# Kernel tuning notes

Hardware: AMD Instinct MI355X
Metric: run time of the kernel (lower is better)

## Reference

```python
import jax, jax.numpy as jnp
import numpy as np

B, S, D, H, E = 4, 2048, 256, 8, 65536
HD = D // H  # head_dim = 32


def _layernorm(x, g, b, eps=1e-5):
    mu = jnp.mean(x, axis=-1, keepdims=True)
    var = jnp.var(x, axis=-1, keepdims=True)
    return (x - mu) * jax.lax.rsqrt(var + eps) * g + b


def setup_inputs() -> dict:
    key = jax.random.key(0)
    ks = jax.random.split(key, 16)
    sd = 1.0 / np.sqrt(D)
    inp = {
        "x": jax.random.normal(ks[0], (B, S, D), jnp.float32),
        "adj_mask": jax.random.uniform(ks[1], (B, S, S)) < 0.05,  # ~32 neighbors/node
        "edge_attr": jax.random.normal(ks[2], (E,), jnp.float32),
        "edge_index": jax.random.randint(ks[3], (2, E), 0, S),
        "ln1_g": jnp.ones((D,), jnp.float32),
        "ln1_b": jnp.zeros((D,), jnp.float32),
        "wq": jax.random.normal(ks[4], (D, D), jnp.float32) * sd,
        "bq": jnp.zeros((D,), jnp.float32),
        "wk": jax.random.normal(ks[5], (D, D), jnp.float32) * sd,
        "bk": jnp.zeros((D,), jnp.float32),
        "wv": jax.random.normal(ks[6], (D, D), jnp.float32) * sd,
        "bv": jnp.zeros((D,), jnp.float32),
        "wo": jax.random.normal(ks[7], (D, D), jnp.float32) * sd,
        "bo": jnp.zeros((D,), jnp.float32),
        "ln2_g": jnp.ones((D,), jnp.float32),
        "ln2_b": jnp.zeros((D,), jnp.float32),
        "w1": jax.random.normal(ks[8], (4 * D, D), jnp.float32) * sd,
        "b1": jnp.zeros((4 * D,), jnp.float32),
        "w2": jax.random.normal(ks[9], (D, 4 * D), jnp.float32) * (1.0 / np.sqrt(4 * D)),
        "b2": jnp.zeros((D,), jnp.float32),
    }
    return inp


def reference(x, adj_mask, edge_attr, edge_index,
              ln1_g, ln1_b, wq, bq, wk, bk, wv, bv, wo, bo,
              ln2_g, ln2_b, w1, b1, w2, b2):
    residual = x
    nx = _layernorm(x, ln1_g, ln1_b)
    # projections (torch Linear: y = x W^T + b)
    q = nx @ wq.T + bq
    k = nx @ wk.T + bk
    v = nx @ wv.T + bv
    # (B,S,D) -> (B,H,S,HD)
    q = q.reshape(B, S, H, HD).transpose(0, 2, 1, 3)
    k = k.reshape(B, S, H, HD).transpose(0, 2, 1, 3)
    v = v.reshape(B, S, H, HD).transpose(0, 2, 1, 3)
    scores = jnp.einsum("bhqd,bhkd->bhqk", q, k) / np.sqrt(HD)
    scores = jnp.where(adj_mask[:, None, :, :], scores, -1e9)
    # edge-attr bias: scatter clipped attr into (S,S), gated per-batch by adj_mask,
    # broadcast over heads (replaces the nested python loop)
    clipped = jnp.clip(edge_attr, -5.0, 5.0)
    bias2d = jnp.zeros((S, S), scores.dtype).at[edge_index[0], edge_index[1]].set(clipped)
    scores = scores + jnp.where(adj_mask, bias2d[None, :, :], 0.0)[:, None, :, :]
    attn = jax.nn.softmax(scores, axis=-1)
    ctx = jnp.einsum("bhqk,bhkd->bhqd", attn, v)
    ctx = ctx.transpose(0, 2, 1, 3).reshape(B, S, D)
    x = residual + (ctx @ wo.T + bo)
    # MLP block (exact GELU, like torch nn.GELU())
    n2 = _layernorm(x, ln2_g, ln2_b)
    h = jax.nn.gelu(n2 @ w1.T + b1, approximate=False)
    x = x + (h @ w2.T + b2)
    return x
```

## Files before the change

### kernel.cpp

```cpp
#include <hip/hip_runtime.h>
#include <stdint.h>

#define S 2048
#define D 256
#define H 8
#define HD 32
#define E_EDGES 65536
#define DFF 1024
#define M_TOK 8192
#define CAP 512
#define QKVN 768

typedef __attribute__((ext_vector_type(8))) short s16x8;
typedef __attribute__((ext_vector_type(8))) unsigned short u16x8;
typedef __attribute__((ext_vector_type(4))) unsigned short u16x4v;
typedef __attribute__((ext_vector_type(4))) float f32x4;

__device__ __forceinline__ float b2f(unsigned short u){
  union { unsigned int i; float f; } x; x.i = ((unsigned int)u) << 16; return x.f;
}
__device__ __forceinline__ unsigned short f2b(float f){
  union { float f; unsigned int i; } x; x.f = f;
  unsigned int r = x.i + 0x7fffu + ((x.i >> 16) & 1u);
  return (unsigned short)(r >> 16);
}
__device__ __forceinline__ void gload_lds16(const void* g, void* l) {
  __builtin_amdgcn_global_load_lds(
      (const __attribute__((address_space(1))) unsigned int*)g,
      (__attribute__((address_space(3))) unsigned int*)l, 16, 0, 0);
}

__global__ __launch_bounds__(256) void prep_kernel(
    const float* __restrict__ wq, const float* __restrict__ wk,
    const float* __restrict__ wv, const float* __restrict__ wo,
    const float* __restrict__ w1, const float* __restrict__ w2,
    const float* __restrict__ bq, const float* __restrict__ bk,
    const float* __restrict__ bv,
    unsigned short* __restrict__ wqkvb, unsigned short* __restrict__ wob,
    unsigned short* __restrict__ w1b, unsigned short* __restrict__ w2b,
    float* __restrict__ bqkv)
{
  const int i = blockIdx.x * 256 + threadIdx.x;
  const float* src; unsigned short* dst; int off;
  if      (i <  16384) { src = wq; dst = wqkvb;            off = i; }
  else if (i <  32768) { src = wk; dst = wqkvb +  65536;   off = i -  16384; }
  else if (i <  49152) { src = wv; dst = wqkvb + 131072;   off = i -  32768; }
  else if (i <  65536) { src = wo; dst = wob;              off = i -  49152; }
  else if (i < 131072) { src = w1; dst = w1b;              off = i -  65536; }
  else                 { src = w2; dst = w2b;              off = i - 131072; }
  const float4 v = ((const float4*)src)[off];
  unsigned short o[4] = { f2b(v.x), f2b(v.y), f2b(v.z), f2b(v.w) };
  *(uint2*)(dst + (size_t)off * 4) = *(const uint2*)o;
  if      (i <  64) ((float4*)bqkv)[i]       = ((const float4*)bq)[i];
  else if (i < 128) ((float4*)bqkv)[i - 64]  = ((const float4*)bk)[i - 64],  ((float4*)bqkv)[i] = ((const float4*)bk)[i - 64];
}

__global__ __launch_bounds__(192) void bias_kernel(
    const float* __restrict__ bq, const float* __restrict__ bk,
    const float* __restrict__ bv, float* __restrict__ bqkv)
{
  const int i = threadIdx.x;
  if      (i <  64) ((float4*)bqkv)[i] = ((const float4*)bq)[i];
  else if (i < 128) ((float4*)bqkv)[i] = ((const float4*)bk)[i - 64];
  else              ((float4*)bqkv)[i] = ((const float4*)bv)[i - 128];
}

__global__ __launch_bounds__(256) void ln_kernel(
    const float* __restrict__ xf,
    const float* __restrict__ g, const float* __restrict__ bt,
    unsigned short* __restrict__ out)
{
  const int wave = threadIdx.x >> 6;
  const int lane = threadIdx.x & 63;
  const int row = blockIdx.x * 4 + wave;
  const size_t base = (size_t)row * D + lane * 4;
  const float4 u = *(const float4*)(xf + base);
  float v[4] = { u.x, u.y, u.z, u.w };
  float s  = v[0]+v[1]+v[2]+v[3];
  float s2 = v[0]*v[0]+v[1]*v[1]+v[2]*v[2]+v[3]*v[3];
  #pragma unroll
  for (int off=32; off>=1; off>>=1){ s += __shfl_xor(s,off,64); s2 += __shfl_xor(s2,off,64); }
  const float mu  = s * (1.f/D);
  const float var = s2 * (1.f/D) - mu*mu;
  const float rs  = 1.f / sqrtf(var + 1e-5f);
  #pragma unroll
  for (int j=0;j<4;++j){
    const int c = lane*4 + j;
    const float y = (v[j]-mu)*rs*g[c] + bt[c];
    out[(size_t)row*D + c] = f2b(y);
  }
}

template<int BM, int BN, int WR, int WC>
__global__ __launch_bounds__(256) void gemm_lds(
    const unsigned short* __restrict__ A,
    const unsigned short* __restrict__ W,
    const float* __restrict__ bias,
    unsigned short* __restrict__ outb,
    float* __restrict__ outf,
    const float* __restrict__ resf,
    int M, int N, int K, int act)
{
  constexpr int WM = BM / WR, WN = BN / WC;
  constexpr int MI = WM / 16, NI = WN / 16;
  __shared__ unsigned short As[2][BM * 32];
  __shared__ unsigned short Bs[2][BN * 32];
  const int tid  = threadIdx.x;
  const int wave = tid >> 6;
  const int lane = tid & 63;
  const int wr = wave / WC, wc = wave % WC;
  const int m0 = blockIdx.y * BM;
  const int n0 = blockIdx.x * BN;
  const int ldr = lane >> 2;
  const int ldc = (lane & 3) * 8;
  const int fr = lane & 15;
  const int kf = (lane >> 4) * 8;
  f32x4 acc[MI][NI];
  #pragma unroll
  for (int i=0;i<MI;++i)
    #pragma unroll
    for (int j=0;j<NI;++j)
      #pragma unroll
      for (int r=0;r<4;++r) acc[i][j][r] = 0.f;

  auto stage = [&](int buf, int k0) {
    #pragma unroll
    for (int c = wave; c < BM/16; c += 4)
      gload_lds16(A + (size_t)(m0 + c*16 + ldr)*K + k0 + ldc, &As[buf][c*512]);
    #pragma unroll
    for (int c = wave; c < BN/16; c += 4)
      gload_lds16(W + (size_t)(n0 + c*16 + ldr)*K + k0 + ldc, &Bs[buf][c*512]);
  };

  stage(0, 0);
  __syncthreads();
  int cur = 0;
  for (int k0 = 0; k0 < K; k0 += 32) {
    if (k0 + 32 < K) stage(cur ^ 1, k0 + 32);
    s16x8 af[MI], bf[NI];
    #pragma unroll
    for (int i = 0; i < MI; ++i) af[i] = *(const s16x8*)&As[cur][(wr*WM + i*16 + fr)*32 + kf];
    #pragma unroll
    for (int j = 0; j < NI; ++j) bf[j] = *(const s16x8*)&Bs[cur][(wc*WN + j*16 + fr)*32 + kf];
    #pragma unroll
    for (int i = 0; i < MI; ++i)
      #pragma unroll
      for (int j = 0; j < NI; ++j)
        acc[i][j] = __builtin_amdgcn_mfma_f32_16x16x32_bf16(af[i], bf[j], acc[i][j], 0, 0, 0);
    __syncthreads();
    cur ^= 1;
  }
  const int rbase = (lane >> 4) * 4;
  #pragma unroll
  for (int j = 0; j < NI; ++j) {
    const int col = n0 + wc*WN + j*16 + fr;
    const float bvl = bias[col];
    #pragma unroll
    for (int i = 0; i < MI; ++i) {
      #pragma unroll
      for (int r = 0; r < 4; ++r) {
        const int row = m0 + wr*WM + i*16 + rbase + r;
        const size_t off = (size_t)row * N + col;
        float vv = acc[i][j][r] + bvl;
        if (act) vv = 0.5f * vv * (1.0f + erff(vv * 0.70710678118654752f));
        if (resf) vv += resf[off];
        if (outb) outb[off] = f2b(vv);
        if (outf) outf[off] = vv;
      }
    }
  }
}

__global__ __launch_bounds__(256) void zero_kernel(uint4* __restrict__ p, int n4) {
  int i = blockIdx.x * 256 + threadIdx.x;
  if (i < n4) { uint4 z; z.x=0; z.y=0; z.z=0; z.w=0; p[i] = z; }
}
__global__ __launch_bounds__(256) void scatter_kernel(
    const int* __restrict__ ei, const float* __restrict__ attr,
    unsigned int* __restrict__ packed)
{
  int e = blockIdx.x * 256 + threadIdx.x;
  if (e >= E_EDGES) return;
  int r = ei[e], c = ei[E_EDGES + e];
  float v = attr[e];
  v = fminf(5.f, fmaxf(-5.f, v));
  unsigned int pk = (((unsigned int)e) << 16) | (unsigned int)f2b(v);
  atomicMax(&packed[(size_t)r * S + c], pk);
}

__global__ __launch_bounds__(256) void attn_kernel(
    const unsigned short* __restrict__ qkv,
    const int* __restrict__ mask,
    const unsigned int* __restrict__ packed,
    unsigned short* __restrict__ ctx)
{
  __shared__ unsigned short nidx[CAP];
  __shared__ float nbias[CAP];
  __shared__ float sc[CAP*9];
  __shared__ float qs[D];
  __shared__ float red[4*D];
  __shared__ float rsum[H];
  __shared__ int wtot[4], wbase[4], cnt_s;
  const int t = threadIdx.x;
  const int wave = t >> 6, lane = t & 63;
  const int bqi = blockIdx.x;
  const int b = bqi >> 11;
  const int qrow = bqi & (S-1);
  qs[t] = b2f(qkv[(size_t)bqi * QKVN + t]);

  const int* mrow = mask + (size_t)bqi * S;
  const uint4 ma = *(const uint4*)(mrow + t*8);
  const uint4 mb = *(const uint4*)(mrow + t*8 + 4);
  unsigned int mv[8] = { ma.x, ma.y, ma.z, ma.w, mb.x, mb.y, mb.z, mb.w };
  int mycnt = 0;
  #pragma unroll
  for (int j = 0; j < 8; ++j) mycnt += mv[j] ? 1 : 0;
  int inc = mycnt;
  #pragma unroll
  for (int off=1; off<64; off<<=1){ int y = __shfl_up(inc, off, 64); if (lane >= off) inc += y; }
  if (lane == 63) wtot[wave] = inc;
  __syncthreads();
  if (t == 0) { int ss=0; for (int w=0; w<4; ++w){ wbase[w]=ss; ss+=wtot[w]; } cnt_s = ss; }
  __syncthreads();
  int pos = wbase[wave] + inc - mycnt;
  #pragma unroll
  for (int j = 0; j < 8; ++j) {
    if (mv[j]) {
      if (pos < CAP) nidx[pos] = (unsigned short)(t*8 + j);
      ++pos;
    }
  }
  __syncthreads();
  int cnt = cnt_s; if (cnt > CAP) cnt = CAP;
  const int cnt_pad = (cnt + 31) & ~31;
  for (int i = cnt + t; i < cnt_pad; i += 256) nidx[i] = 0;

  for (int i = t; i < cnt; i += 256) {
    unsigned int pkv = packed[(size_t)qrow * S + nidx[i]];
    nbias[i] = b2f((unsigned short)(pkv & 0xffffu));
  }
  __syncthreads();

  const int hh = lane >> 3;
  const int d4 = (lane & 7) * 4;
  const float scale = 0.17677669529663687f;
  float q4[4];
  #pragma unroll
  for (int j = 0; j < 4; ++j) q4[j] = qs[hh*HD + d4 + j];
  const size_t rowbase = (size_t)b * S * QKVN;

  for (int n0 = wave*8; n0 < cnt_pad; n0 += 32) {
    u16x4v kv[8];
    #pragma unroll
    for (int u = 0; u < 8; ++u)
      kv[u] = *(const u16x4v*)(qkv + rowbase + (size_t)nidx[n0+u]*QKVN + 256 + lane*4);
    #pragma unroll
    for (int u = 0; u < 8; ++u) {
      float p = q4[0]*b2f(kv[u][0]) + q4[1]*b2f(kv[u][1]) + q4[2]*b2f(kv[u][2]) + q4[3]*b2f(kv[u][3]);
      p += __shfl_xor(p, 1, 64);
      p += __shfl_xor(p, 2, 64);
      p += __shfl_xor(p, 4, 64);
      if ((lane & 7) == 0) {
        const int n = n0 + u;
        sc[n*9 + hh] = (n < cnt) ? p * scale + nbias[n] : 0.f;
      }
    }
  }
  __syncthreads();

  if (cnt > 0) {
    const int h = t >> 5, dd = t & 31;
    float m = -1e30f;
    for (int n = dd; n < cnt; n += 32) m = fmaxf(m, sc[n*9 + h]);
    #pragma unroll
    for (int off=16; off>=1; off>>=1) m = fmaxf(m, __shfl_xor(m, off, 64));
    float sum = 0.f;
    for (int n = dd; n < cnt; n += 32) {
      float e = __expf(sc[n*9 + h] - m);
      sc[n*9 + h] = e;
      sum += e;
    }
    #pragma unroll
    for (int off=16; off>=1; off>>=1) sum += __shfl_xor(sum, off, 64);
    if (dd == 0) rsum[h] = 1.f / sum;
  }
  __syncthreads();

  float a4[4] = {0.f, 0.f, 0.f, 0.f};
  if (cnt > 0) {
    for (int n0 = wave*8; n0 < cnt_pad; n0 += 32) {
      u16x4v vv[8];
      #pragma unroll
      for (int u = 0; u < 8; ++u)
        vv[u] = *(const u16x4v*)(qkv + rowbase + (size_t)nidx[n0+u]*QKVN + 512 + lane*4);
      #pragma unroll
      for (int u = 0; u < 8; ++u) {
        const float p = sc[(n0+u)*9 + hh];
        a4[0] += p * b2f(vv[u][0]);
        a4[1] += p * b2f(vv[u][1]);
        a4[2] += p * b2f(vv[u][2]);
        a4[3] += p * b2f(vv[u][3]);
      }
    }
    const float rinv = rsum[hh];
    #pragma unroll
    for (int j = 0; j < 4; ++j) a4[j] *= rinv;
  } else {
    for (int n = wave; n < S; n += 4) {
      const unsigned short* vrow = qkv + rowbase + (size_t)n * QKVN + 512;
      u16x4v vv = *(const u16x4v*)(vrow + lane*4);
      a4[0] += b2f(vv[0]); a4[1] += b2f(vv[1]); a4[2] += b2f(vv[2]); a4[3] += b2f(vv[3]);
    }
    #pragma unroll
    for (int j = 0; j < 4; ++j) a4[j] *= (1.f / S);
  }
  #pragma unroll
  for (int j = 0; j < 4; ++j) red[wave*D + lane*4 + j] = a4[j];
  __syncthreads();
  float outv = red[t] + red[D + t] + red[2*D + t] + red[3*D + t];
  ctx[(size_t)bqi * D + t] = f2b(outv);
}

extern "C" void kernel_launch(void* const* d_in, const int* in_sizes, int n_in,
                              void* d_out, int out_size, void* d_ws, size_t ws_size,
                              hipStream_t stream) {
  const float*          x    = (const float*)d_in[0];
  const int*            mask = (const int*)d_in[1];
  const float*          eat  = (const float*)d_in[2];
  const int*            eidx = (const int*)d_in[3];
  const float*          ln1g = (const float*)d_in[4];
  const float*          ln1b = (const float*)d_in[5];
  const float*          wq   = (const float*)d_in[6];
  const float*          bq   = (const float*)d_in[7];
  const float*          wk   = (const float*)d_in[8];
  const float*          bk   = (const float*)d_in[9];
  const float*          wv   = (const float*)d_in[10];
  const float*          bv   = (const float*)d_in[11];
  const float*          wo   = (const float*)d_in[12];
  const float*          bo   = (const float*)d_in[13];
  const float*          ln2g = (const float*)d_in[14];
  const float*          ln2b = (const float*)d_in[15];
  const float*          w1   = (const float*)d_in[16];
  const float*          b1   = (const float*)d_in[17];
  const float*          w2   = (const float*)d_in[18];
  const float*          b2   = (const float*)d_in[19];
  float* out = (float*)d_out;

  char* ws = (char*)d_ws;
  unsigned short* nx   = (unsigned short*)ws;
  unsigned short* qkv  = nx + (size_t)M_TOK*D;
  unsigned short* cx   = qkv + (size_t)M_TOK*QKVN;
  float*          x1   = (float*)(cx + (size_t)M_TOK*D);
  unsigned int*   pk   = (unsigned int*)(x1 + (size_t)M_TOK*D);
  unsigned short* wqkvb= (unsigned short*)(pk + (size_t)S*S);
  unsigned short* wob  = wqkvb + (size_t)QKVN*D;
  unsigned short* w1b  = wob + (size_t)D*D;
  unsigned short* w2b  = w1b + (size_t)DFF*D;
  float*          bqkv = (float*)(w2b + (size_t)D*DFF);
  unsigned short* hb   = qkv;
  unsigned short* n2   = nx;

  prep_kernel<<<768, 256, 0, stream>>>(wq, wk, wv, wo, w1, w2, bq, bk, bv,
                                       wqkvb, wob, w1b, w2b, bqkv);
  bias_kernel<<<1, 192, 0, stream>>>(bq, bk, bv, bqkv);
  zero_kernel<<<(S*S/4 + 255)/256, 256, 0, stream>>>((uint4*)pk, S*S/4);
  scatter_kernel<<<E_EDGES/256, 256, 0, stream>>>(eidx, eat, pk);
  ln_kernel<<<M_TOK/4, 256, 0, stream>>>(x, ln1g, ln1b, nx);
  gemm_lds<64,128,1,4><<<dim3(QKVN/128, M_TOK/64), 256, 0, stream>>>(nx, wqkvb, bqkv, qkv, nullptr, nullptr, M_TOK, QKVN, D, 0);
  attn_kernel<<<M_TOK, 256, 0, stream>>>(qkv, mask, pk, cx);
  gemm_lds<64,64,2,2><<<dim3(D/64, M_TOK/64), 256, 0, stream>>>(cx, wob, bo, nullptr, x1, x, M_TOK, D, D, 0);
  ln_kernel<<<M_TOK/4, 256, 0, stream>>>(x1, ln2g, ln2b, n2);
  gemm_lds<128,128,2,2><<<dim3(DFF/128, M_TOK/128), 256, 0, stream>>>(n2, w1b, b1, hb, nullptr, nullptr, M_TOK, DFF, D, 1);
  gemm_lds<64,64,2,2><<<dim3(D/64, M_TOK/64), 256, 0, stream>>>(hb, w2b, b2, nullptr, out, x1, M_TOK, D, DFF, 0);
}
```

Before: 177.6 us.

## Remap attention lanes to neighbor-by-head with per-thread full head dot products

Changes the attention thread mapping so each lane handles one neighbor and one head, doing a full 32-element dot product with 16-byte K/V loads instead of 4-element partials followed by shuffle reductions. Precomputed byte offsets per neighbor are stored in shared memory, and the PV accumulation keeps 32 accumulators per lane, reduced with cross-lane shuffles at the end. Softmax normalization moves to the final output sum. This also drops the redundant bias copy from the prep kernel. It trades shuffle and score-store overhead for higher register use (q32 and a32 arrays), which may lower occupancy, plus a 32-step shuffle reduction.

```diff
diff --git a/kernel.cpp b/kernel.cpp
--- a/kernel.cpp
+++ b/kernel.cpp
@@ -34,11 +34,8 @@
     const float* __restrict__ wq, const float* __restrict__ wk,
     const float* __restrict__ wv, const float* __restrict__ wo,
     const float* __restrict__ w1, const float* __restrict__ w2,
-    const float* __restrict__ bq, const float* __restrict__ bk,
-    const float* __restrict__ bv,
     unsigned short* __restrict__ wqkvb, unsigned short* __restrict__ wob,
-    unsigned short* __restrict__ w1b, unsigned short* __restrict__ w2b,
-    float* __restrict__ bqkv)
+    unsigned short* __restrict__ w1b, unsigned short* __restrict__ w2b)
 {
   const int i = blockIdx.x * 256 + threadIdx.x;
   const float* src; unsigned short* dst; int off;
@@ -51,8 +48,6 @@
   const float4 v = ((const float4*)src)[off];
   unsigned short o[4] = { f2b(v.x), f2b(v.y), f2b(v.z), f2b(v.w) };
   *(uint2*)(dst + (size_t)off * 4) = *(const uint2*)o;
-  if      (i <  64) ((float4*)bqkv)[i]       = ((const float4*)bq)[i];
-  else if (i < 128) ((float4*)bqkv)[i - 64]  = ((const float4*)bk)[i - 64],  ((float4*)bqkv)[i] = ((const float4*)bk)[i - 64];
 }
 
 __global__ __launch_bounds__(192) void bias_kernel(
@@ -195,9 +190,9 @@
     unsigned short* __restrict__ ctx)
 {
   __shared__ unsigned short nidx[CAP];
+  __shared__ unsigned int noff[CAP];
   __shared__ float nbias[CAP];
   __shared__ float sc[CAP*9];
-  __shared__ float qs[D];
   __shared__ float red[4*D];
   __shared__ float rsum[H];
   __shared__ int wtot[4], wbase[4], cnt_s;
@@ -206,7 +201,6 @@
   const int bqi = blockIdx.x;
   const int b = bqi >> 11;
   const int qrow = bqi & (S-1);
-  qs[t] = b2f(qkv[(size_t)bqi * QKVN + t]);
 
   const int* mrow = mask + (size_t)bqi * S;
   const uint4 ma = *(const uint4*)(mrow + t*8);
@@ -233,38 +227,47 @@
   __syncthreads();
   int cnt = cnt_s; if (cnt > CAP) cnt = CAP;
   const int cnt_pad = (cnt + 31) & ~31;
-  for (int i = cnt + t; i < cnt_pad; i += 256) nidx[i] = 0;
+  for (int i = cnt + t; i < cnt_pad; i += 256) { nidx[i] = 0; noff[i] = 512u; nbias[i] = 0.f; }
 
   for (int i = t; i < cnt; i += 256) {
-    unsigned int pkv = packed[(size_t)qrow * S + nidx[i]];
+    const unsigned int ni = nidx[i];
+    noff[i] = ni * 1536u + 512u;
+    unsigned int pkv = packed[(size_t)qrow * S + ni];
     nbias[i] = b2f((unsigned short)(pkv & 0xffffu));
   }
   __syncthreads();
 
-  const int hh = lane >> 3;
-  const int d4 = (lane & 7) * 4;
+  const int ns = lane >> 3;
+  const int hh = lane & 7;
   const float scale = 0.17677669529663687f;
-  float q4[4];
-  #pragma unroll
-  for (int j = 0; j < 4; ++j) q4[j] = qs[hh*HD + d4 + j];
-  const size_t rowbase = (size_t)b * S * QKVN;
+  const char* kbase = (const char*)(qkv + (size_t)b * S * QKVN) + hh * 64;
+
+  float q32[32];
+  {
+    const u16x8* qp = (const u16x8*)(qkv + (size_t)bqi * QKVN + hh * HD);
+    #pragma unroll
+    for (int c = 0; c < 4; ++c) {
+      u16x8 qv = qp[c];
+      #pragma unroll
+      for (int j = 0; j < 8; ++j) q32[c*8+j] = b2f(qv[j]);
+    }
+  }
 
   for (int n0 = wave*8; n0 < cnt_pad; n0 += 32) {
-    u16x4v kv[8];
-    #pragma unroll
-    for (int u = 0; u < 8; ++u)
-      kv[u] = *(const u16x4v*)(qkv + rowbase + (size_t)nidx[n0+u]*QKVN + 256 + lane*4);
-    #pragma unroll
-    for (int u = 0; u < 8; ++u) {
-      float p = q4[0]*b2f(kv[u][0]) + q4[1]*b2f(kv[u][1]) + q4[2]*b2f(kv[u][2]) + q4[3]*b2f(kv[u][3]);
-      p += __shfl_xor(p, 1, 64);
-      p += __shfl_xor(p, 2, 64);
-      p += __shfl_xor(p, 4, 64);
-      if ((lane & 7) == 0) {
-        const int n = n0 + u;
-        sc[n*9 + hh] = (n < cnt) ? p * scale + nbias[n] : 0.f;
-      }
-    }
+    const int n = n0 + ns;
+    const unsigned int off = noff[n];
+    const u16x8* kp = (const u16x8*)(kbase + off);
+    u16x8 kv0 = kp[0], kv1 = kp[1], kv2 = kp[2], kv3 = kp[3];
+    float d0 = 0.f, d1 = 0.f, d2 = 0.f, d3 = 0.f;
+    #pragma unroll
+    for (int j = 0; j < 8; ++j) {
+      d0 += q32[j]    * b2f(kv0[j]);
+      d1 += q32[8+j]  * b2f(kv1[j]);
+      d2 += q32[16+j] * b2f(kv2[j]);
+      d3 += q32[24+j] * b2f(kv3[j]);
+    }
+    const float scv = ((d0+d1)+(d2+d3)) * scale + nbias[n];
+    sc[n*9 + hh] = (n < cnt) ? scv : 0.f;
   }
   __syncthreads();
 
@@ -286,38 +289,48 @@
   }
   __syncthreads();
 
-  float a4[4] = {0.f, 0.f, 0.f, 0.f};
   if (cnt > 0) {
+    float a32[32];
+    #pragma unroll
+    for (int j = 0; j < 32; ++j) a32[j] = 0.f;
     for (int n0 = wave*8; n0 < cnt_pad; n0 += 32) {
-      u16x4v vv[8];
-      #pragma unroll
-      for (int u = 0; u < 8; ++u)
-        vv[u] = *(const u16x4v*)(qkv + rowbase + (size_t)nidx[n0+u]*QKVN + 512 + lane*4);
-      #pragma unroll
-      for (int u = 0; u < 8; ++u) {
-        const float p = sc[(n0+u)*9 + hh];
-        a4[0] += p * b2f(vv[u][0]);
-        a4[1] += p * b2f(vv[u][1]);
-        a4[2] += p * b2f(vv[u][2]);
-        a4[3] += p * b2f(vv[u][3]);
+      const int n = n0 + ns;
+      const unsigned int off = noff[n];
+      const u16x8* vp = (const u16x8*)(kbase + off + 512);
+      u16x8 v0 = vp[0], v1 = vp[1], v2 = vp[2], v3 = vp[3];
+      const float p = sc[n*9 + hh];
+      #pragma unroll
+      for (int j = 0; j < 8; ++j) {
+        a32[j]    += p * b2f(v0[j]);
+        a32[8+j]  += p * b2f(v1[j]);
+        a32[16+j] += p * b2f(v2[j]);
+        a32[24+j] += p * b2f(v3[j]);
       }
     }
-    const float rinv = rsum[hh];
-    #pragma unroll
-    for (int j = 0; j < 4; ++j) a4[j] *= rinv;
+    #pragma unroll
+    for (int mm = 8; mm <= 32; mm <<= 1)
+      #pragma unroll
+      for (int j = 0; j < 32; ++j) a32[j] += __shfl_xor(a32[j], mm, 64);
+    if (ns == 0) {
+      #pragma unroll
+      for (int c = 0; c < 8; ++c) {
+        f32x4 w4 = { a32[c*4], a32[c*4+1], a32[c*4+2], a32[c*4+3] };
+        *(f32x4*)&red[wave*D + hh*HD + c*4] = w4;
+      }
+    }
   } else {
+    float a4[4] = {0.f, 0.f, 0.f, 0.f};
     for (int n = wave; n < S; n += 4) {
-      const unsigned short* vrow = qkv + rowbase + (size_t)n * QKVN + 512;
-      u16x4v vv = *(const u16x4v*)(vrow + lane*4);
+      const u16x4v vv = *(const u16x4v*)((const char*)(qkv + (size_t)b*S*QKVN) + (size_t)n*1536 + 1024 + lane*8);
       a4[0] += b2f(vv[0]); a4[1] += b2f(vv[1]); a4[2] += b2f(vv[2]); a4[3] += b2f(vv[3]);
     }
     #pragma unroll
     for (int j = 0; j < 4; ++j) a4[j] *= (1.f / S);
-  }
-  #pragma unroll
-  for (int j = 0; j < 4; ++j) red[wave*D + lane*4 + j] = a4[j];
-  __syncthreads();
-  float outv = red[t] + red[D + t] + red[2*D + t] + red[3*D + t];
+    *(f32x4*)&red[wave*D + lane*4] = *(f32x4*)a4;
+    if (t < 8) rsum[t] = 1.f;
+  }
+  __syncthreads();
+  const float outv = (red[t] + red[D + t] + red[2*D + t] + red[3*D + t]) * rsum[t >> 5];
   ctx[(size_t)bqi * D + t] = f2b(outv);
 }
 
@@ -360,8 +373,7 @@
   unsigned short* hb   = qkv;
   unsigned short* n2   = nx;
 
-  prep_kernel<<<768, 256, 0, stream>>>(wq, wk, wv, wo, w1, w2, bq, bk, bv,
-                                       wqkvb, wob, w1b, w2b, bqkv);
+  prep_kernel<<<768, 256, 0, stream>>>(wq, wk, wv, wo, w1, w2, wqkvb, wob, w1b, w2b);
   bias_kernel<<<1, 192, 0, stream>>>(bq, bk, bv, bqkv);
   zero_kernel<<<(S*S/4 + 255)/256, 256, 0, stream>>>((uint4*)pk, S*S/4);
   scatter_kernel<<<E_EDGES/256, 256, 0, stream>>>(eidx, eat, pk);
```

Result: slower. 187.2 us (+5.4%).

## Split neighbor-list build into CSR kernel and store K/V as fp32 rows

Applied to the files above, without the earlier changes.

Moves mask compaction and edge-bias lookup out of the attention kernel into a separate csr_kernel that writes packed (index, bias) entries per query. The QKV GEMM now writes Q as bf16 and K/V as fp32 into separate buffers, so attention reads 16-byte float4 gathers with no bf16 conversion. Neighbor capacity drops from 512 to 192, which shrinks shared memory and should raise occupancy, but it truncates any row with more than 192 neighbors. The workspace is reorganized with aliased buffers, and the fp32 K/V doubles gather bandwidth per neighbor.

```diff
diff --git a/kernel.cpp b/kernel.cpp
--- a/kernel.cpp
+++ b/kernel.cpp
@@ -8,7 +8,7 @@
 #define E_EDGES 65536
 #define DFF 1024
 #define M_TOK 8192
-#define CAP 512
+#define CAPR 192
 #define QKVN 768
 
 typedef __attribute__((ext_vector_type(8))) short s16x8;
@@ -34,11 +34,8 @@
     const float* __restrict__ wq, const float* __restrict__ wk,
     const float* __restrict__ wv, const float* __restrict__ wo,
     const float* __restrict__ w1, const float* __restrict__ w2,
-    const float* __restrict__ bq, const float* __restrict__ bk,
-    const float* __restrict__ bv,
     unsigned short* __restrict__ wqkvb, unsigned short* __restrict__ wob,
-    unsigned short* __restrict__ w1b, unsigned short* __restrict__ w2b,
-    float* __restrict__ bqkv)
+    unsigned short* __restrict__ w1b, unsigned short* __restrict__ w2b)
 {
   const int i = blockIdx.x * 256 + threadIdx.x;
   const float* src; unsigned short* dst; int off;
@@ -51,8 +48,6 @@
   const float4 v = ((const float4*)src)[off];
   unsigned short o[4] = { f2b(v.x), f2b(v.y), f2b(v.z), f2b(v.w) };
   *(uint2*)(dst + (size_t)off * 4) = *(const uint2*)o;
-  if      (i <  64) ((float4*)bqkv)[i]       = ((const float4*)bq)[i];
-  else if (i < 128) ((float4*)bqkv)[i - 64]  = ((const float4*)bk)[i - 64],  ((float4*)bqkv)[i] = ((const float4*)bk)[i - 64];
 }
 
 __global__ __launch_bounds__(192) void bias_kernel(
@@ -96,8 +91,9 @@
     const unsigned short* __restrict__ A,
     const unsigned short* __restrict__ W,
     const float* __restrict__ bias,
-    unsigned short* __restrict__ outb,
+    unsigned short* __restrict__ outb, int obN,
     float* __restrict__ outf,
+    float* __restrict__ outkv,
     const float* __restrict__ resf,
     int M, int N, int K, int act)
 {
@@ -164,8 +160,9 @@
         float vv = acc[i][j][r] + bvl;
         if (act) vv = 0.5f * vv * (1.0f + erff(vv * 0.70710678118654752f));
         if (resf) vv += resf[off];
-        if (outb) outb[off] = f2b(vv);
+        if (outb && col < obN) outb[(size_t)row * obN + col] = f2b(vv);
         if (outf) outf[off] = vv;
+        if (outkv && col >= 256) outkv[(size_t)row * 512 + (col - 256)] = vv;
       }
     }
   }
@@ -188,26 +185,16 @@
   atomicMax(&packed[(size_t)r * S + c], pk);
 }
 
-__global__ __launch_bounds__(256) void attn_kernel(
-    const unsigned short* __restrict__ qkv,
-    const int* __restrict__ mask,
-    const unsigned int* __restrict__ packed,
-    unsigned short* __restrict__ ctx)
-{
-  __shared__ unsigned short nidx[CAP];
-  __shared__ float nbias[CAP];
-  __shared__ float sc[CAP*9];
-  __shared__ float qs[D];
-  __shared__ float red[4*D];
-  __shared__ float rsum[H];
+__global__ __launch_bounds__(256) void csr_kernel(
+    const int* __restrict__ mask, const unsigned int* __restrict__ packed,
+    unsigned int* __restrict__ csr, int* __restrict__ cnts)
+{
+  __shared__ unsigned short nidx[CAPR];
   __shared__ int wtot[4], wbase[4], cnt_s;
   const int t = threadIdx.x;
   const int wave = t >> 6, lane = t & 63;
   const int bqi = blockIdx.x;
-  const int b = bqi >> 11;
   const int qrow = bqi & (S-1);
-  qs[t] = b2f(qkv[(size_t)bqi * QKVN + t]);
-
   const int* mrow = mask + (size_t)bqi * S;
   const uint4 ma = *(const uint4*)(mrow + t*8);
   const uint4 mb = *(const uint4*)(mrow + t*8 + 4);
@@ -226,43 +213,71 @@
   #pragma unroll
   for (int j = 0; j < 8; ++j) {
     if (mv[j]) {
-      if (pos < CAP) nidx[pos] = (unsigned short)(t*8 + j);
+      if (pos < CAPR) nidx[pos] = (unsigned short)(t*8 + j);
       ++pos;
     }
   }
   __syncthreads();
-  int cnt = cnt_s; if (cnt > CAP) cnt = CAP;
+  int cnt = cnt_s; if (cnt > CAPR) cnt = CAPR;
   const int cnt_pad = (cnt + 31) & ~31;
-  for (int i = cnt + t; i < cnt_pad; i += 256) nidx[i] = 0;
-
-  for (int i = t; i < cnt; i += 256) {
-    unsigned int pkv = packed[(size_t)qrow * S + nidx[i]];
-    nbias[i] = b2f((unsigned short)(pkv & 0xffffu));
-  }
-  __syncthreads();
+  for (int i = t; i < cnt_pad; i += 256) {
+    unsigned int e = 0;
+    if (i < cnt) {
+      const unsigned int ni = nidx[i];
+      e = (ni << 16) | (packed[(size_t)qrow * S + ni] & 0xffffu);
+    }
+    csr[(size_t)bqi * CAPR + i] = e;
+  }
+  if (t == 0) cnts[bqi] = cnt;
+}
+
+__global__ __launch_bounds__(256) void attn_kernel(
+    const unsigned short* __restrict__ qb,
+    const float* __restrict__ kvf,
+    const unsigned int* __restrict__ csr,
+    const int* __restrict__ cnts,
+    unsigned short* __restrict__ ctx)
+{
+  __shared__ unsigned int nle[CAPR];
+  __shared__ float sc[CAPR*9];
+  __shared__ float red[4*D];
+  __shared__ float rsum[H];
+  const int t = threadIdx.x;
+  const int wave = t >> 6, lane = t & 63;
+  const int bqi = blockIdx.x;
+  const int b = bqi >> 11;
+  const char* kvb = (const char*)(kvf + (size_t)b * S * 512);
+
+  const int cnt = cnts[bqi];
+  const int cnt_pad = (cnt + 31) & ~31;
+  for (int i = t; i < cnt_pad; i += 256) nle[i] = csr[(size_t)bqi * CAPR + i];
 
   const int hh = lane >> 3;
-  const int d4 = (lane & 7) * 4;
   const float scale = 0.17677669529663687f;
   float q4[4];
-  #pragma unroll
-  for (int j = 0; j < 4; ++j) q4[j] = qs[hh*HD + d4 + j];
-  const size_t rowbase = (size_t)b * S * QKVN;
+  {
+    const u16x4v qv = *(const u16x4v*)(qb + (size_t)bqi * D + lane * 4);
+    #pragma unroll
+    for (int j = 0; j < 4; ++j) q4[j] = b2f(qv[j]);
+  }
+  __syncthreads();
 
   for (int n0 = wave*8; n0 < cnt_pad; n0 += 32) {
-    u16x4v kv[8];
+    unsigned int e[8]; float4 kv[8];
+    #pragma unroll
+    for (int u = 0; u < 8; ++u) e[u] = nle[n0 + u];
     #pragma unroll
     for (int u = 0; u < 8; ++u)
-      kv[u] = *(const u16x4v*)(qkv + rowbase + (size_t)nidx[n0+u]*QKVN + 256 + lane*4);
+      kv[u] = *(const float4*)(kvb + (size_t)((e[u] >> 16) * 2048u) + lane*16);
     #pragma unroll
     for (int u = 0; u < 8; ++u) {
-      float p = q4[0]*b2f(kv[u][0]) + q4[1]*b2f(kv[u][1]) + q4[2]*b2f(kv[u][2]) + q4[3]*b2f(kv[u][3]);
+      float p = q4[0]*kv[u].x + q4[1]*kv[u].y + q4[2]*kv[u].z + q4[3]*kv[u].w;
       p += __shfl_xor(p, 1, 64);
       p += __shfl_xor(p, 2, 64);
       p += __shfl_xor(p, 4, 64);
       if ((lane & 7) == 0) {
         const int n = n0 + u;
-        sc[n*9 + hh] = (n < cnt) ? p * scale + nbias[n] : 0.f;
+        sc[n*9 + hh] = (n < cnt) ? fmaf(p, scale, b2f((unsigned short)(e[u] & 0xffffu))) : 0.f;
       }
     }
   }
@@ -276,9 +291,9 @@
     for (int off=16; off>=1; off>>=1) m = fmaxf(m, __shfl_xor(m, off, 64));
     float sum = 0.f;
     for (int n = dd; n < cnt; n += 32) {
-      float e = __expf(sc[n*9 + h] - m);
-      sc[n*9 + h] = e;
-      sum += e;
+      float ev = __expf(sc[n*9 + h] - m);
+      sc[n*9 + h] = ev;
+      sum += ev;
     }
     #pragma unroll
     for (int off=16; off>=1; off>>=1) sum += __shfl_xor(sum, off, 64);
@@ -289,35 +304,33 @@
   float a4[4] = {0.f, 0.f, 0.f, 0.f};
   if (cnt > 0) {
     for (int n0 = wave*8; n0 < cnt_pad; n0 += 32) {
-      u16x4v vv[8];
+      unsigned int e[8]; float4 vv[8];
+      #pragma unroll
+      for (int u = 0; u < 8; ++u) e[u] = nle[n0 + u];
       #pragma unroll
       for (int u = 0; u < 8; ++u)
-        vv[u] = *(const u16x4v*)(qkv + rowbase + (size_t)nidx[n0+u]*QKVN + 512 + lane*4);
+        vv[u] = *(const float4*)(kvb + (size_t)((e[u] >> 16) * 2048u) + 1024 + lane*16);
       #pragma unroll
       for (int u = 0; u < 8; ++u) {
         const float p = sc[(n0+u)*9 + hh];
-        a4[0] += p * b2f(vv[u][0]);
-        a4[1] += p * b2f(vv[u][1]);
-        a4[2] += p * b2f(vv[u][2]);
-        a4[3] += p * b2f(vv[u][3]);
+        a4[0] += p * vv[u].x;
+        a4[1] += p * vv[u].y;
+        a4[2] += p * vv[u].z;
+        a4[3] += p * vv[u].w;
       }
     }
-    const float rinv = rsum[hh];
-    #pragma unroll
-    for (int j = 0; j < 4; ++j) a4[j] *= rinv;
   } else {
     for (int n = wave; n < S; n += 4) {
-      const unsigned short* vrow = qkv + rowbase + (size_t)n * QKVN + 512;
-      u16x4v vv = *(const u16x4v*)(vrow + lane*4);
-      a4[0] += b2f(vv[0]); a4[1] += b2f(vv[1]); a4[2] += b2f(vv[2]); a4[3] += b2f(vv[3]);
+      const float4 vv = *(const float4*)(kvb + (size_t)n * 2048 + 1024 + lane*16);
+      a4[0] += vv.x; a4[1] += vv.y; a4[2] += vv.z; a4[3] += vv.w;
     }
     #pragma unroll
     for (int j = 0; j < 4; ++j) a4[j] *= (1.f / S);
-  }
-  #pragma unroll
-  for (int j = 0; j < 4; ++j) red[wave*D + lane*4 + j] = a4[j];
-  __syncthreads();
-  float outv = red[t] + red[D + t] + red[2*D + t] + red[3*D + t];
+    if (t < 8) rsum[t] = 1.f;
+  }
+  *(f32x4*)&red[wave*D + lane*4] = *(f32x4*)a4;
+  __syncthreads();
+  const float outv = (red[t] + red[D + t] + red[2*D + t] + red[3*D + t]) * rsum[t >> 5];
   ctx[(size_t)bqi * D + t] = f2b(outv);
 }
 
@@ -348,28 +361,35 @@
 
   char* ws = (char*)d_ws;
   unsigned short* nx   = (unsigned short*)ws;
-  unsigned short* qkv  = nx + (size_t)M_TOK*D;
-  unsigned short* cx   = qkv + (size_t)M_TOK*QKVN;
-  float*          x1   = (float*)(cx + (size_t)M_TOK*D);
-  unsigned int*   pk   = (unsigned int*)(x1 + (size_t)M_TOK*D);
-  unsigned short* wqkvb= (unsigned short*)(pk + (size_t)S*S);
+  unsigned short* qb   = (unsigned short*)(ws + (4u<<20));
+  unsigned short* cx   = (unsigned short*)(ws + (8u<<20));
+  float*          x1   = (float*)(ws + (12u<<20));
+  unsigned int*   csr  = (unsigned int*)(ws + (12u<<20));
+  int*            cnts = (int*)(csr + (size_t)M_TOK * CAPR);
+  float*          kvf  = (float*)(ws + (20u<<20));
+  unsigned int*   pk   = (unsigned int*)(ws + (20u<<20));
+  unsigned short* wqkvb= (unsigned short*)(ws + (36u<<20));
   unsigned short* wob  = wqkvb + (size_t)QKVN*D;
   unsigned short* w1b  = wob + (size_t)D*D;
   unsigned short* w2b  = w1b + (size_t)DFF*D;
   float*          bqkv = (float*)(w2b + (size_t)D*DFF);
-  unsigned short* hb   = qkv;
+  unsigned short* hb   = (unsigned short*)kvf;
   unsigned short* n2   = nx;
 
-  prep_kernel<<<768, 256, 0, stream>>>(wq, wk, wv, wo, w1, w2, bq, bk, bv,
-                                       wqkvb, wob, w1b, w2b, bqkv);
+  prep_kernel<<<768, 256, 0, stream>>>(wq, wk, wv, wo, w1, w2, wqkvb, wob, w1b, w2b);
   bias_kernel<<<1, 192, 0, stream>>>(bq, bk, bv, bqkv);
   zero_kernel<<<(S*S/4 + 255)/256, 256, 0, stream>>>((uint4*)pk, S*S/4);
   scatter_kernel<<<E_EDGES/256, 256, 0, stream>>>(eidx, eat, pk);
   ln_kernel<<<M_TOK/4, 256, 0, stream>>>(x, ln1g, ln1b, nx);
-  gemm_lds<64,128,1,4><<<dim3(QKVN/128, M_TOK/64), 256, 0, stream>>>(nx, wqkvb, bqkv, qkv, nullptr, nullptr, M_TOK, QKVN, D, 0);
-  attn_kernel<<<M_TOK, 256, 0, stream>>>(qkv, mask, pk, cx);
-  gemm_lds<64,64,2,2><<<dim3(D/64, M_TOK/64), 256, 0, stream>>>(cx, wob, bo, nullptr, x1, x, M_TOK, D, D, 0);
+  csr_kernel<<<M_TOK, 256, 0, stream>>>(mask, pk, csr, cnts);
+  gemm_lds<64,128,1,4><<<dim3(QKVN/128, M_TOK/64), 256, 0, stream>>>(
+      nx, wqkvb, bqkv, qb, 256, nullptr, kvf, nullptr, M_TOK, QKVN, D, 0);
+  attn_kernel<<<M_TOK, 256, 0, stream>>>(qb, kvf, csr, cnts, cx);
+  gemm_lds<64,64,2,2><<<dim3(D/64, M_TOK/64), 256, 0, stream>>>(
+      cx, wob, bo, nullptr, 0, x1, nullptr, x, M_TOK, D, D, 0);
   ln_kernel<<<M_TOK/4, 256, 0, stream>>>(x1, ln2g, ln2b, n2);
-  gemm_lds<128,128,2,2><<<dim3(DFF/128, M_TOK/128), 256, 0, stream>>>(n2, w1b, b1, hb, nullptr, nullptr, M_TOK, DFF, D, 1);
-  gemm_lds<64,64,2,2><<<dim3(D/64, M_TOK/64), 256, 0, stream>>>(hb, w2b, b2, nullptr, out, x1, M_TOK, D, DFF, 0);
-}
+  gemm_lds<128,128,2,2><<<dim3(DFF/128, M_TOK/128), 256, 0, stream>>>(
+      n2, w1b, b1, hb, DFF, nullptr, nullptr, nullptr, M_TOK, DFF, D, 1);
+  gemm_lds<64,64,2,2><<<dim3(D/64, M_TOK/64), 256, 0, stream>>>(
+      hb, w2b, b2, nullptr, 0, out, nullptr, x1, M_TOK, D, DFF, 0);
+}
```

New measurement: 194.9 us. 1.1x slower.
